# Optimization experiments

Measured on AMD Instinct MI355X. Metric: run time of the kernel, lower is better.

## Reference

```python
import jax, jax.numpy as jnp
import numpy as np


def setup_inputs() -> dict:
    key = jax.random.key(0)
    ks = jax.random.split(key, 5)
    B, H, W, C = 64, 14, 14, 2048
    x = jax.random.normal(ks[0], (B, H, W, C), dtype=jnp.float32)
    # Glorot-ish scaled 1x1 conv weights (stored as [Cin, Cout])
    W1 = jax.random.normal(ks[1], (C, 64), dtype=jnp.float32) * (1.0 / np.sqrt(C))
    W2 = jax.random.normal(ks[2], (64, 16), dtype=jnp.float32) * (1.0 / np.sqrt(64))
    W3 = jax.random.normal(ks[3], (16, 8), dtype=jnp.float32) * (1.0 / np.sqrt(16))
    W4 = jax.random.normal(ks[4], (8, 1), dtype=jnp.float32) * (1.0 / np.sqrt(8))
    return {
        "x": x,
        "W1": W1, "b1": jnp.zeros((64,), jnp.float32),
        "W2": W2, "b2": jnp.zeros((16,), jnp.float32),
        "W3": W3, "b3": jnp.zeros((8,), jnp.float32),
        "W4": W4, "b4": jnp.zeros((1,), jnp.float32),
    }


def reference(x, W1, b1, W2, b2, W3, b3, W4, b4):
    # Dropout is identity at inference time.
    # 1x1 convs == per-pixel matmuls over channel dim.
    h = jax.nn.relu(jnp.einsum('bhwc,cd->bhwd', x, W1) + b1)   # [B,H,W,64]
    h = jax.nn.relu(jnp.einsum('bhwc,cd->bhwd', h, W2) + b2)   # [B,H,W,16]
    h = jax.nn.relu(jnp.einsum('bhwc,cd->bhwd', h, W3) + b3)   # [B,H,W,8]
    a = jax.nn.sigmoid(jnp.einsum('bhwc,cd->bhwd', h, W4) + b4)  # [B,H,W,1]
    # 'upsample' frozen ones-conv == broadcast of a over 2048 channels.
    gap_features = jnp.mean(a * x, axis=(1, 2))  # [B, 2048]
    gap_mask = jnp.mean(a, axis=(1, 2))          # [B, 1] (same value for all 2048 chans)
    return gap_features / gap_mask               # [B, 2048]
```

## Files before the change

### kernel.cpp

```cpp
#include <hip/hip_runtime.h>
#include <math.h>

#define NPIX 12544
#define CIN  2048
#define NB   64
#define PPIX 196
#define PSPLIT 7
#define PCHUNK 28

typedef short  bf16x8 __attribute__((ext_vector_type(8)));
typedef float  f32x4  __attribute__((ext_vector_type(4)));

__device__ inline unsigned short f2bf(float f) {
    unsigned int u = __float_as_uint(f);
    u = (u + 0x7fffu + ((u >> 16) & 1u)) >> 16;
    return (unsigned short)u;
}

__global__ __launch_bounds__(256) void conv_w1(
    const float* __restrict__ W1, unsigned short* __restrict__ W1t)
{
    const int id = blockIdx.x * 256 + threadIdx.x;
    const int n = id >> 11;
    const int k = id & 2047;
    W1t[id] = f2bf(W1[k * 64 + n]);
}

__global__ __launch_bounds__(512) void attn_scores_mfma(
    const float* __restrict__ x, const unsigned short* __restrict__ W1t,
    const float* __restrict__ b1,
    const float* __restrict__ W2, const float* __restrict__ b2,
    const float* __restrict__ W3, const float* __restrict__ b3,
    const float* __restrict__ W4, const float* __restrict__ b4,
    float* __restrict__ a_out)
{
    __shared__ float part[8][16][68];
    __shared__ float h1s[16][68];
    __shared__ float h2s[16][16];
    __shared__ float h3s[16][8];

    const int t    = threadIdx.x;
    const int wv   = t >> 6;
    const int lane = t & 63;
    const int l15  = lane & 15;
    const int q    = lane >> 4;
    const size_t pix0 = (size_t)blockIdx.x * 16;

    const float* xr = x + (pix0 + l15) * (size_t)CIN + wv * 256 + q * 8;
    const unsigned short* wr = W1t + (size_t)l15 * CIN + wv * 256 + q * 8;

    f32x4 acc[4] = {{0,0,0,0},{0,0,0,0},{0,0,0,0},{0,0,0,0}};

#pragma unroll 2
    for (int k0 = 0; k0 < 256; k0 += 32) {
        float4 xa = *(const float4*)(xr + k0);
        float4 xb = *(const float4*)(xr + k0 + 4);
        bf16x8 af;
        af[0] = (short)f2bf(xa.x); af[1] = (short)f2bf(xa.y);
        af[2] = (short)f2bf(xa.z); af[3] = (short)f2bf(xa.w);
        af[4] = (short)f2bf(xb.x); af[5] = (short)f2bf(xb.y);
        af[6] = (short)f2bf(xb.z); af[7] = (short)f2bf(xb.w);
#pragma unroll
        for (int ct = 0; ct < 4; ++ct) {
            bf16x8 bfr = *(const bf16x8*)(wr + (size_t)ct * 16 * CIN + k0);
            acc[ct] = __builtin_amdgcn_mfma_f32_16x16x32_bf16(af, bfr, acc[ct], 0, 0, 0);
        }
    }

#pragma unroll
    for (int ct = 0; ct < 4; ++ct)
#pragma unroll
        for (int r = 0; r < 4; ++r)
            part[wv][q * 4 + r][ct * 16 + l15] = acc[ct][r];
    __syncthreads();

    const int p = t >> 4;
    const int j = t & 15;

    if (t < 256) {
        const int c0 = j * 4;
        f32x4 s = {0, 0, 0, 0};
#pragma unroll
        for (int w = 0; w < 8; ++w) s += *(const f32x4*)&part[w][p][c0];
        const f32x4 bb = *(const f32x4*)(b1 + c0);
        f32x4 hv;
#pragma unroll
        for (int i = 0; i < 4; ++i) hv[i] = fmaxf(s[i] + bb[i], 0.f);
        *(f32x4*)&h1s[p][c0] = hv;
    }
    __syncthreads();

    if (t < 256) {
        float s = b2[j];
#pragma unroll
        for (int k = 0; k < 64; ++k) s = fmaf(h1s[p][k], W2[k * 16 + j], s);
        h2s[p][j] = fmaxf(s, 0.f);
    }
    __syncthreads();

    if (t < 256 && j < 8) {
        float s = b3[j];
#pragma unroll
        for (int k = 0; k < 16; ++k) s = fmaf(h2s[p][k], W3[k * 8 + j], s);
        h3s[p][j] = fmaxf(s, 0.f);
    }
    __syncthreads();

    if (t < 256 && j == 0) {
        float z = b4[0];
#pragma unroll
        for (int k = 0; k < 8; ++k) z = fmaf(h3s[p][k], W4[k], z);
        a_out[pix0 + p] = 1.f / (1.f + expf(-z));
    }
}

__global__ __launch_bounds__(256) void gap_partial(
    const float* __restrict__ x, const float* __restrict__ a,
    float* __restrict__ part)
{
    const int b  = blockIdx.y;
    const int pz = blockIdx.z;
    const int c0 = (blockIdx.x * 256 + threadIdx.x) * 4;
    const float* xb = x + ((size_t)b * PPIX + pz * PCHUNK) * CIN + c0;
    const float* ab = a + b * PPIX + pz * PCHUNK;

    float4 s0 = {0,0,0,0}, s1 = {0,0,0,0};
#pragma unroll 4
    for (int p = 0; p < PCHUNK; p += 2) {
        const float a0 = ab[p], a1 = ab[p + 1];
        const float4 v0 = *(const float4*)(xb + (size_t)p * CIN);
        const float4 v1 = *(const float4*)(xb + (size_t)(p + 1) * CIN);
        s0.x = fmaf(a0, v0.x, s0.x); s0.y = fmaf(a0, v0.y, s0.y);
        s0.z = fmaf(a0, v0.z, s0.z); s0.w = fmaf(a0, v0.w, s0.w);
        s1.x = fmaf(a1, v1.x, s1.x); s1.y = fmaf(a1, v1.y, s1.y);
        s1.z = fmaf(a1, v1.z, s1.z); s1.w = fmaf(a1, v1.w, s1.w);
    }
    float4 r;
    r.x = s0.x + s1.x; r.y = s0.y + s1.y; r.z = s0.z + s1.z; r.w = s0.w + s1.w;
    *(float4*)(part + ((size_t)pz * NB + b) * CIN + c0) = r;
}

__global__ __launch_bounds__(512) void gap_final(
    const float* __restrict__ a, const float* __restrict__ part,
    float* __restrict__ out)
{
    __shared__ float red[512];
    const int b = blockIdx.x, t = threadIdx.x;
    red[t] = (t < PPIX) ? a[b * PPIX + t] : 0.f;
    __syncthreads();
#pragma unroll
    for (int s = 256; s > 0; s >>= 1) {
        if (t < s) red[t] += red[t + s];
        __syncthreads();
    }
    const float inv = 1.f / red[0];
    const int c0 = t * 4;
    float4 acc = {0, 0, 0, 0};
#pragma unroll
    for (int z = 0; z < PSPLIT; ++z) {
        const float4 pv = *(const float4*)(part + ((size_t)z * NB + b) * CIN + c0);
        acc.x += pv.x; acc.y += pv.y; acc.z += pv.z; acc.w += pv.w;
    }
    float4 r;
    r.x = acc.x * inv; r.y = acc.y * inv; r.z = acc.z * inv; r.w = acc.w * inv;
    *(float4*)(out + (size_t)b * CIN + c0) = r;
}

extern "C" void kernel_launch(void* const* d_in, const int* in_sizes, int n_in,
                              void* d_out, int out_size, void* d_ws, size_t ws_size,
                              hipStream_t stream)
{
    const float* x  = (const float*)d_in[0];
    const float* W1 = (const float*)d_in[1];
    const float* b1 = (const float*)d_in[2];
    const float* W2 = (const float*)d_in[3];
    const float* b2 = (const float*)d_in[4];
    const float* W3 = (const float*)d_in[5];
    const float* b3 = (const float*)d_in[6];
    const float* W4 = (const float*)d_in[7];
    const float* b4 = (const float*)d_in[8];
    float* out = (float*)d_out;

    unsigned short* W1t = (unsigned short*)d_ws;
    float* a    = (float*)((char*)d_ws + (256 << 10));
    float* part = (float*)((char*)d_ws + (512 << 10));

    conv_w1<<<512, 256, 0, stream>>>(W1, W1t);
    attn_scores_mfma<<<NPIX / 16, 512, 0, stream>>>(x, W1t, b1, W2, b2, W3, b3, W4, b4, a);
    gap_partial<<<dim3(2, NB, PSPLIT), 256, 0, stream>>>(x, a, part);
    gap_final<<<NB, 512, 0, stream>>>(a, part, out);
}
```

Measured before the change: 213.8 us.

## Prefetch x and W1 fragments into registers in MFMA scoring and GAP kernels

The MFMA attention-score kernel now loads all x rows up front and double-buffers the W1 bf16 fragments across k-steps, raising memory-level parallelism and adding an occupancy hint of two blocks per CU. The GAP partial kernel halves its pixel chunk and doubles the split, then issues all chunk loads before the FMAs. The goal is to hide global memory latency on these bandwidth-bound passes over x. The cost is higher register pressure, which may limit occupancy, and twice as much partial-sum traffic into gap_final.

```diff
diff --git a/kernel.cpp b/kernel.cpp
--- a/kernel.cpp
+++ b/kernel.cpp
@@ -5,8 +5,8 @@
 #define CIN  2048
 #define NB   64
 #define PPIX 196
-#define PSPLIT 7
-#define PCHUNK 28
+#define PSPLIT 14
+#define PCHUNK 14
 
 typedef short  bf16x8 __attribute__((ext_vector_type(8)));
 typedef float  f32x4  __attribute__((ext_vector_type(4)));
@@ -26,7 +26,7 @@
     W1t[id] = f2bf(W1[k * 64 + n]);
 }
 
-__global__ __launch_bounds__(512) void attn_scores_mfma(
+__global__ __launch_bounds__(512, 2) void attn_scores_mfma(
     const float* __restrict__ x, const unsigned short* __restrict__ W1t,
     const float* __restrict__ b1,
     const float* __restrict__ W2, const float* __restrict__ b2,
@@ -51,19 +51,49 @@
 
     f32x4 acc[4] = {{0,0,0,0},{0,0,0,0},{0,0,0,0},{0,0,0,0}};
 
-#pragma unroll 2
-    for (int k0 = 0; k0 < 256; k0 += 32) {
-        float4 xa = *(const float4*)(xr + k0);
-        float4 xb = *(const float4*)(xr + k0 + 4);
+    float4 xv[16];
+#pragma unroll
+    for (int i = 0; i < 4; ++i) {
+        xv[2*i]   = *(const float4*)(xr + 32*i);
+        xv[2*i+1] = *(const float4*)(xr + 32*i + 4);
+    }
+    bf16x8 wA[4], wB[4];
+#pragma unroll
+    for (int ct = 0; ct < 4; ++ct)
+        wA[ct] = *(const bf16x8*)(wr + (size_t)ct * 16 * CIN);
+
+#pragma unroll
+    for (int i = 0; i < 8; ++i) {
+        if (i < 4) {
+            xv[8+2*i] = *(const float4*)(xr + 32*(i+4));
+            xv[9+2*i] = *(const float4*)(xr + 32*(i+4) + 4);
+        }
+        if (i < 7) {
+            if ((i & 1) == 0) {
+#pragma unroll
+                for (int ct = 0; ct < 4; ++ct)
+                    wB[ct] = *(const bf16x8*)(wr + (size_t)ct * 16 * CIN + 32*(i+1));
+            } else {
+#pragma unroll
+                for (int ct = 0; ct < 4; ++ct)
+                    wA[ct] = *(const bf16x8*)(wr + (size_t)ct * 16 * CIN + 32*(i+1));
+            }
+        }
+        const float4 xa = xv[(2*i) & 15];
+        const float4 xb = xv[(2*i+1) & 15];
         bf16x8 af;
         af[0] = (short)f2bf(xa.x); af[1] = (short)f2bf(xa.y);
         af[2] = (short)f2bf(xa.z); af[3] = (short)f2bf(xa.w);
         af[4] = (short)f2bf(xb.x); af[5] = (short)f2bf(xb.y);
         af[6] = (short)f2bf(xb.z); af[7] = (short)f2bf(xb.w);
-#pragma unroll
-        for (int ct = 0; ct < 4; ++ct) {
-            bf16x8 bfr = *(const bf16x8*)(wr + (size_t)ct * 16 * CIN + k0);
-            acc[ct] = __builtin_amdgcn_mfma_f32_16x16x32_bf16(af, bfr, acc[ct], 0, 0, 0);
+        if ((i & 1) == 0) {
+#pragma unroll
+            for (int ct = 0; ct < 4; ++ct)
+                acc[ct] = __builtin_amdgcn_mfma_f32_16x16x32_bf16(af, wA[ct], acc[ct], 0, 0, 0);
+        } else {
+#pragma unroll
+            for (int ct = 0; ct < 4; ++ct)
+                acc[ct] = __builtin_amdgcn_mfma_f32_16x16x32_bf16(af, wB[ct], acc[ct], 0, 0, 0);
         }
     }
 
@@ -124,16 +154,22 @@
     const float* xb = x + ((size_t)b * PPIX + pz * PCHUNK) * CIN + c0;
     const float* ab = a + b * PPIX + pz * PCHUNK;
 
+    float av[PCHUNK];
+#pragma unroll
+    for (int p = 0; p < PCHUNK; ++p) av[p] = ab[p];
+
+    float4 xv[PCHUNK];
+#pragma unroll
+    for (int p = 0; p < PCHUNK; ++p)
+        xv[p] = *(const float4*)(xb + (size_t)p * CIN);
+
     float4 s0 = {0,0,0,0}, s1 = {0,0,0,0};
-#pragma unroll 4
+#pragma unroll
     for (int p = 0; p < PCHUNK; p += 2) {
-        const float a0 = ab[p], a1 = ab[p + 1];
-        const float4 v0 = *(const float4*)(xb + (size_t)p * CIN);
-        const float4 v1 = *(const float4*)(xb + (size_t)(p + 1) * CIN);
-        s0.x = fmaf(a0, v0.x, s0.x); s0.y = fmaf(a0, v0.y, s0.y);
-        s0.z = fmaf(a0, v0.z, s0.z); s0.w = fmaf(a0, v0.w, s0.w);
-        s1.x = fmaf(a1, v1.x, s1.x); s1.y = fmaf(a1, v1.y, s1.y);
-        s1.z = fmaf(a1, v1.z, s1.z); s1.w = fmaf(a1, v1.w, s1.w);
+        s0.x = fmaf(av[p], xv[p].x, s0.x);   s0.y = fmaf(av[p], xv[p].y, s0.y);
+        s0.z = fmaf(av[p], xv[p].z, s0.z);   s0.w = fmaf(av[p], xv[p].w, s0.w);
+        s1.x = fmaf(av[p+1], xv[p+1].x, s1.x); s1.y = fmaf(av[p+1], xv[p+1].y, s1.y);
+        s1.z = fmaf(av[p+1], xv[p+1].z, s1.z); s1.w = fmaf(av[p+1], xv[p+1].w, s1.w);
     }
     float4 r;
     r.x = s0.x + s1.x; r.y = s0.y + s1.y; r.z = s0.z + s1.z; r.w = s0.w + s1.w;
```

Result: faster. 209.4 us (-2.1%).
